# Optimization experiments

Measured on AMD Instinct MI355X. Metric: run time of the kernel, lower is better.

The kernel has to match this reference:

```python
import jax, jax.numpy as jnp
import numpy as np


def _conv2d(x, w, b):
    # x: [B,C,H,W], w: [O,I,kh,kw] (SAME padding, stride 1)
    y = jax.lax.conv_general_dilated(x, w, (1, 1), 'SAME',
                                     dimension_numbers=('NCHW', 'OIHW', 'NCHW'))
    return y + b[None, :, None, None]


def _conv1x1(x, w, b):
    # w: [O,C], b: [O]
    return jnp.einsum('oc,bchw->bohw', w, x) + b[None, :, None, None]


def _attention(xq, xkv, w, b):
    # w: [3,C,C] (q,k,v), b: [3,C]. Tokens = spatial positions, features = channels.
    B, C, H, W = xq.shape
    q = _conv1x1(xq, w[0], b[0]).reshape(B, C, H * W).transpose(0, 2, 1)   # [B,HW,C]
    k = _conv1x1(xkv, w[1], b[1]).reshape(B, C, H * W).transpose(0, 2, 1)
    v = _conv1x1(xkv, w[2], b[2]).reshape(B, C, H * W).transpose(0, 2, 1)
    scale = 1.0 / jnp.sqrt(jnp.asarray(C, xq.dtype))  # d_k = channels
    a = jax.nn.softmax(jnp.einsum('bnc,bmc->bnm', q, k) * scale, axis=-1)  # [B,HW,HW]
    out = jnp.einsum('bnm,bmc->bnc', a, v).transpose(0, 2, 1).reshape(B, C, H, W)
    return out + xq


def _cell(x, h, c, w, b):
    gates = _conv2d(jnp.concatenate([x, h], axis=1), w, b)
    i, f, o, g = jnp.split(gates, 4, axis=1)
    i, f, o, g = jax.nn.sigmoid(i), jax.nn.sigmoid(f), jax.nn.sigmoid(o), jnp.tanh(g)
    c_new = f * c + i * g
    h_new = o * jnp.tanh(c_new)
    return h_new, c_new


def setup_inputs() -> dict:
    key = jax.random.key(0)
    ks = iter(jax.random.split(key, 32))
    B, T, Cin, H, W = 2, 3, 1, 32, 32
    HID, L, K, OUT = 64, 2, 3, 1
    s = 0.02
    d = {
        'x1_seq': jax.random.normal(next(ks), (B, T, Cin, H, W), jnp.float32),
        'x2_seq': jax.random.normal(next(ks), (B, T, Cin, H, W), jnp.float32),
        # ConvLSTM gate convs: layer0 in = Cin+HID, layer1 in = 2*HID, per stream
        'conv1_w0': jax.random.normal(next(ks), (4 * HID, Cin + HID, K, K)) * s,
        'conv1_b0': jnp.zeros((4 * HID,)),
        'conv1_w1': jax.random.normal(next(ks), (4 * HID, 2 * HID, K, K)) * s,
        'conv1_b1': jnp.zeros((4 * HID,)),
        'conv2_w0': jax.random.normal(next(ks), (4 * HID, Cin + HID, K, K)) * s,
        'conv2_b0': jnp.zeros((4 * HID,)),
        'conv2_w1': jax.random.normal(next(ks), (4 * HID, 2 * HID, K, K)) * s,
        'conv2_b1': jnp.zeros((4 * HID,)),
        # attention 1x1 convs, stacked [L, 3(q/k/v), HID, HID]
        'sah_w': jax.random.normal(next(ks), (L, 3, HID, HID)) * s,
        'sah_b': jnp.zeros((L, 3, HID)),
        'sac_w': jax.random.normal(next(ks), (L, 3, HID, HID)) * s,
        'sac_b': jnp.zeros((L, 3, HID)),
        'cah_w': jax.random.normal(next(ks), (L, 3, HID, HID)) * s,
        'cah_b': jnp.zeros((L, 3, HID)),
        'cac_w': jax.random.normal(next(ks), (L, 3, HID, HID)) * s,
        'cac_b': jnp.zeros((L, 3, HID)),
        # decoder
        'dec_w1': jax.random.normal(next(ks), (HID, HID, 3, 3)) * s,
        'dec_b1': jnp.zeros((HID,)),
        'dec_w2': jax.random.normal(next(ks), (OUT, HID, 3, 3)) * s,
        'dec_b2': jnp.zeros((OUT,)),
        'future_steps': 4,
    }
    return d


def reference(x1_seq, x2_seq,
              conv1_w0, conv1_b0, conv1_w1, conv1_b1,
              conv2_w0, conv2_b0, conv2_w1, conv2_b1,
              sah_w, sah_b, sac_w, sac_b, cah_w, cah_b, cac_w, cac_b,
              dec_w1, dec_b1, dec_w2, dec_b2, future_steps):
    B, T, _, H, W = x1_seq.shape
    HID = sah_w.shape[-1]
    L = sah_w.shape[0]
    cw1 = [(conv1_w0, conv1_b0), (conv1_w1, conv1_b1)]
    cw2 = [(conv2_w0, conv2_b0), (conv2_w1, conv2_b1)]

    def decoder(h):
        return _conv2d(jax.nn.relu(_conv2d(h, dec_w1, dec_b1)), dec_w2, dec_b2)

    z = jnp.zeros((B, HID, H, W), x1_seq.dtype)
    h1s, c1s = [z] * L, [z] * L
    h2s, c2s = [z] * L, [z] * L

    def step(x1_t, x2_t, h1s, c1s, h2s, c2s):
        h1s, c1s, h2s, c2s = list(h1s), list(c1s), list(h2s), list(c2s)
        for l in range(L):
            h1, c1 = _cell(x1_t, h1s[l], c1s[l], *cw1[l])
            h2, c2 = _cell(x2_t, h2s[l], c2s[l], *cw2[l])
            h1 = _attention(h1, h1, sah_w[l], sah_b[l])
            c1 = _attention(c1, c1, sac_w[l], sac_b[l])
            h2 = _attention(h2, h2, sah_w[l], sah_b[l])
            c2 = _attention(c2, c2, sac_w[l], sac_b[l])
            tag_h1, tag_c1 = h1, c1
            h1 = _attention(h1, h2, cah_w[l], cah_b[l])
            c1 = _attention(c1, c2, cac_w[l], cac_b[l])
            h2 = _attention(h2, tag_h1, cah_w[l], cah_b[l])
            c2 = _attention(c2, tag_c1, cac_w[l], cac_b[l])
            h1s[l], c1s[l], h2s[l], c2s[l] = h1, c1, h2, c2
            x1_t, x2_t = h1, h2
        return h1s, c1s, h2s, c2s

    warm1, warm2 = [], []
    for t in range(T):
        h1s, c1s, h2s, c2s = step(x1_seq[:, t], x2_seq[:, t], h1s, c1s, h2s, c2s)
        if t < T - 1:
            warm1.append(h1s[-1])
            warm2.append(h2s[-1])
    pred_warm1 = jnp.stack([decoder(h) for h in warm1], axis=1)
    pred_warm2 = jnp.stack([decoder(h) for h in warm2], axis=1)

    preds1, preds2 = [], []
    for _ in range(int(future_steps)):
        p1 = decoder(h1s[-1])
        p2 = decoder(h2s[-1])
        preds1.append(p1)
        preds2.append(p2)
        h1s, c1s, h2s, c2s = step(p1, p2, h1s, c1s, h2s, c2s)
    preds1 = jnp.stack(preds1, axis=1)
    preds2 = jnp.stack(preds2, axis=1)
    return preds1, preds2, pred_warm1, pred_warm2
```

## Files before the change

kernel.cpp:

```cpp
#include <hip/hip_runtime.h>
#include <math.h>

#define BB 2
#define HIDC 64
#define HWN 1024

struct TWArgs { const float* src[5]; float* dst[5]; int icn9[5]; int osh[5]; };

__global__ __launch_bounds__(256) void transpose_w(TWArgs a) {
  const int arr = blockIdx.y;
  const int icn9 = a.icn9[arr], osh = a.osh[arr];
  const int ocn = 1 << osh;
  const float* s = a.src[arr];
  float* d = a.dst[arr];
  const int n = icn9 << osh;
  for (int i = blockIdx.x * 256 + threadIdx.x; i < n; i += gridDim.x * 256) {
    int oc = i & (ocn - 1), tt = i >> osh;
    d[i] = s[(size_t)oc * icn9 + tt];
  }
}

struct CellArgs {
  const float* x[2]; long xbs;
  const float* h[2]; const float* c[2];
  const float* w[2]; const float* bias[2];
  float* ho[2]; float* co[2];
};

template<int CX>
__global__ __launch_bounds__(512) void cell_kernel(CellArgs a) {
  constexpr int CT = CX + HIDC;
  constexpr int CH = (CT + 1) / 2;
  __shared__ float sIn[CT * 48];
  __shared__ float sGa[256 * 17];
  __shared__ float sGb[256 * 17];
  const int tile = blockIdx.x;
  const int b = blockIdx.y;
  const int st = blockIdx.z;
  const int ty0 = (tile >> 3) << 2, tx0 = (tile & 7) << 2;
  const float* xp = a.x[st] + (size_t)b * a.xbs;
  const float* hp = a.h[st] + (size_t)b * HIDC * HWN;

  for (int idx = threadIdx.x; idx < CT * 36; idx += 512) {
    int ic = idx / 36, pos = idx - ic * 36;
    int iy = pos / 6, ix = pos - iy * 6;
    int gy = ty0 - 1 + iy, gx = tx0 - 1 + ix;
    float v = 0.f;
    if ((unsigned)gy < 32u && (unsigned)gx < 32u) {
      v = (ic < CX) ? xp[ic * HWN + gy * 32 + gx]
                    : hp[(ic - CX) * HWN + gy * 32 + gx];
    }
    sIn[ic * 48 + iy * 8 + ix] = v;
  }
  __syncthreads();

  const int oc = threadIdx.x & 255;
  const int hh = threadIdx.x >> 8;
  const int icb = hh ? CH : 0, ice = hh ? CT : CH;
  float acc[16];
#pragma unroll
  for (int p = 0; p < 16; ++p) acc[p] = 0.f;
  const float* wp = a.w[st];
  for (int ic = icb; ic < ice; ++ic) {
    float w9[9];
#pragma unroll
    for (int t = 0; t < 9; ++t) w9[t] = wp[(ic * 9 + t) * 256 + oc];
    float in[36];
#pragma unroll
    for (int iy = 0; iy < 6; ++iy) {
      float4 v4 = *(const float4*)&sIn[ic * 48 + iy * 8];
      float2 v2 = *(const float2*)&sIn[ic * 48 + iy * 8 + 4];
      in[iy * 6 + 0] = v4.x; in[iy * 6 + 1] = v4.y; in[iy * 6 + 2] = v4.z;
      in[iy * 6 + 3] = v4.w; in[iy * 6 + 4] = v2.x; in[iy * 6 + 5] = v2.y;
    }
#pragma unroll
    for (int ky = 0; ky < 3; ++ky)
#pragma unroll
      for (int kx = 0; kx < 3; ++kx) {
        const float wv = w9[ky * 3 + kx];
#pragma unroll
        for (int py = 0; py < 4; ++py)
#pragma unroll
          for (int px = 0; px < 4; ++px)
            acc[py * 4 + px] += wv * in[(py + ky) * 6 + (px + kx)];
      }
  }
  float* sGh = hh ? sGb : sGa;
#pragma unroll
  for (int p = 0; p < 16; ++p) sGh[oc * 17 + p] = acc[p];
  __syncthreads();

  const float* cp = a.c[st] + (size_t)b * HIDC * HWN;
  float* hop = a.ho[st] + (size_t)b * HIDC * HWN;
  float* cop = a.co[st] + (size_t)b * HIDC * HWN;
  const float* bias = a.bias[st];
  for (int idx = threadIdx.x; idx < HIDC * 16; idx += 512) {
    int hc = idx >> 4, p = idx & 15;
    float gi = sGa[hc * 17 + p]         + sGb[hc * 17 + p]         + bias[hc];
    float gf = sGa[(hc + 64) * 17 + p]  + sGb[(hc + 64) * 17 + p]  + bias[hc + 64];
    float go = sGa[(hc + 128) * 17 + p] + sGb[(hc + 128) * 17 + p] + bias[hc + 128];
    float gg = sGa[(hc + 192) * 17 + p] + sGb[(hc + 192) * 17 + p] + bias[hc + 192];
    gi = 1.f / (1.f + expf(-gi));
    gf = 1.f / (1.f + expf(-gf));
    go = 1.f / (1.f + expf(-go));
    gg = tanhf(gg);
    int off = hc * HWN + (ty0 + (p >> 2)) * 32 + tx0 + (p & 3);
    float cn = gf * cp[off] + gi * gg;
    cop[off] = cn;
    hop[off] = go * tanhf(cn);
  }
}

struct QkvArgs {
  const float* xq[4]; const float* xkv[4];
  const float* w[4]; const float* bias[4];
  float* Q; float* K; float* V;
};

__global__ __launch_bounds__(256) void qkv_kernel(QkvArgs a) {
  __shared__ float sWt[64 * 68];
  const int ptile = blockIdx.x, b = blockIdx.y;
  const int attn = blockIdx.z / 3, proj = blockIdx.z % 3;
  const float* x = (proj == 0 ? a.xq[attn] : a.xkv[attn]) + (size_t)b * HIDC * HWN;
  const float* w = a.w[attn] + proj * 64 * 64;
  const float* bias = a.bias[attn] + proj * 64;
  float* dst = (proj == 0 ? a.Q : (proj == 1 ? a.K : a.V)) +
               ((size_t)attn * BB + b) * HWN * HIDC;
  for (int i = threadIdx.x; i < 4096; i += 256) {
    int o = i >> 6, c = i & 63;
    sWt[c * 68 + o] = w[i];
  }
  __syncthreads();
  const int pq = threadIdx.x & 63, og = threadIdx.x >> 6;
  const int p0 = ptile * 64 + pq;
  float acc[16];
#pragma unroll
  for (int k = 0; k < 16; ++k) acc[k] = bias[og * 16 + k];
  for (int c = 0; c < 64; ++c) {
    float xv = x[c * HWN + p0];
#pragma unroll
    for (int k = 0; k < 16; k += 4) {
      float4 wv = *(const float4*)&sWt[c * 68 + og * 16 + k];
      acc[k+0] += xv * wv.x; acc[k+1] += xv * wv.y;
      acc[k+2] += xv * wv.z; acc[k+3] += xv * wv.w;
    }
  }
  float* d = dst + (size_t)p0 * HIDC + og * 16;
#pragma unroll
  for (int k = 0; k < 16; k += 4) {
    float4 v; v.x = acc[k]; v.y = acc[k+1]; v.z = acc[k+2]; v.w = acc[k+3];
    *(float4*)&d[k] = v;
  }
}

struct AttnPArgs { const float* Q; const float* K; const float* V; float* pbuf; };

__global__ __launch_bounds__(256) void attn_part(AttnPArgs a) {
  __shared__ float sQt[64 * 64];
  __shared__ float sKt[64 * 64];
  __shared__ float sV [64 * 64];
  __shared__ float sPt[64 * 64];
  const int qt = blockIdx.x >> 2, ks = blockIdx.x & 3;
  const int b = blockIdx.y, at = blockIdx.z;
  const size_t base = ((size_t)at * BB + b) * HWN * HIDC;
  const float* Qp = a.Q + base + (size_t)qt * 64 * HIDC;
  const float* Kp = a.K + base;
  const float* Vp = a.V + base;
  const int tid = threadIdx.x;
  {
    const int qr = tid & 63, qc0 = (tid >> 6) * 16;
    const float* q = Qp + qr * HIDC + qc0;
#pragma unroll
    for (int k = 0; k < 16; k += 4) {
      float4 v = *(const float4*)&q[k];
      sQt[(qc0 + k + 0) * 64 + qr] = v.x * 0.125f;
      sQt[(qc0 + k + 1) * 64 + qr] = v.y * 0.125f;
      sQt[(qc0 + k + 2) * 64 + qr] = v.z * 0.125f;
      sQt[(qc0 + k + 3) * 64 + qr] = v.w * 0.125f;
    }
  }
  const int tc = tid & 15, tr = tid >> 4;
  const int j0 = tc * 4, r0 = tr * 4;
  const int kj = tid & 63, kch = (tid >> 6) * 16;
  const int vj = tid >> 2, vc0 = (tid & 3) * 16;
  float m[4], l[4], o[4][4];
#pragma unroll
  for (int i = 0; i < 4; ++i) {
    m[i] = -1e30f; l[i] = 0.f;
    o[i][0] = 0; o[i][1] = 0; o[i][2] = 0; o[i][3] = 0;
  }

  const int ktb = ks * 4;
  float4 kr[4], vr[4];
  {
    const float* kp = Kp + (size_t)(ktb * 64 + kj) * HIDC + kch;
    const float* vp = Vp + (size_t)(ktb * 64 + vj) * HIDC + vc0;
#pragma unroll
    for (int q2 = 0; q2 < 4; ++q2) {
      kr[q2] = *(const float4*)&kp[q2 * 4];
      vr[q2] = *(const float4*)&vp[q2 * 4];
    }
  }

  for (int kk = 0; kk < 4; ++kk) {
    __syncthreads();
#pragma unroll
    for (int q2 = 0; q2 < 4; ++q2) {
      sKt[(kch + q2 * 4 + 0) * 64 + kj] = kr[q2].x;
      sKt[(kch + q2 * 4 + 1) * 64 + kj] = kr[q2].y;
      sKt[(kch + q2 * 4 + 2) * 64 + kj] = kr[q2].z;
      sKt[(kch + q2 * 4 + 3) * 64 + kj] = kr[q2].w;
      int c = vc0 + q2 * 4;
      *(float4*)&sV[vj * 64 + (c ^ ((vj & 7) * 4))] = vr[q2];
    }
    __syncthreads();
    if (kk < 3) {
      const float* kp = Kp + (size_t)((ktb + kk + 1) * 64 + kj) * HIDC + kch;
      const float* vp = Vp + (size_t)((ktb + kk + 1) * 64 + vj) * HIDC + vc0;
#pragma unroll
      for (int q2 = 0; q2 < 4; ++q2) {
        kr[q2] = *(const float4*)&kp[q2 * 4];
        vr[q2] = *(const float4*)&vp[q2 * 4];
      }
    }
    float s[4][4];
#pragma unroll
    for (int i = 0; i < 4; ++i) { s[i][0]=0; s[i][1]=0; s[i][2]=0; s[i][3]=0; }
#pragma unroll 4
    for (int c = 0; c < 64; ++c) {
      float4 q4 = *(const float4*)&sQt[c * 64 + r0];
      float4 k4 = *(const float4*)&sKt[c * 64 + j0];
      s[0][0]+=q4.x*k4.x; s[0][1]+=q4.x*k4.y; s[0][2]+=q4.x*k4.z; s[0][3]+=q4.x*k4.w;
      s[1][0]+=q4.y*k4.x; s[1][1]+=q4.y*k4.y; s[1][2]+=q4.y*k4.z; s[1][3]+=q4.y*k4.w;
      s[2][0]+=q4.z*k4.x; s[2][1]+=q4.z*k4.y; s[2][2]+=q4.z*k4.z; s[2][3]+=q4.z*k4.w;
      s[3][0]+=q4.w*k4.x; s[3][1]+=q4.w*k4.y; s[3][2]+=q4.w*k4.z; s[3][3]+=q4.w*k4.w;
    }
    float mt[4];
#pragma unroll
    for (int i = 0; i < 4; ++i)
      mt[i] = fmaxf(fmaxf(s[i][0], s[i][1]), fmaxf(s[i][2], s[i][3]));
#pragma unroll
    for (int d = 1; d < 16; d <<= 1) {
#pragma unroll
      for (int i = 0; i < 4; ++i) mt[i] = fmaxf(mt[i], __shfl_xor(mt[i], d));
    }
    float al[4];
#pragma unroll
    for (int i = 0; i < 4; ++i) {
      float mn = fmaxf(m[i], mt[i]);
      al[i] = __expf(m[i] - mn);
      m[i] = mn;
      s[i][0] = __expf(s[i][0] - mn); s[i][1] = __expf(s[i][1] - mn);
      s[i][2] = __expf(s[i][2] - mn); s[i][3] = __expf(s[i][3] - mn);
    }
    float ps[4];
#pragma unroll
    for (int i = 0; i < 4; ++i) ps[i] = s[i][0] + s[i][1] + s[i][2] + s[i][3];
#pragma unroll
    for (int d = 1; d < 16; d <<= 1) {
#pragma unroll
      for (int i = 0; i < 4; ++i) ps[i] += __shfl_xor(ps[i], d);
    }
#pragma unroll
    for (int i = 0; i < 4; ++i) {
      l[i] = l[i] * al[i] + ps[i];
      o[i][0] *= al[i]; o[i][1] *= al[i]; o[i][2] *= al[i]; o[i][3] *= al[i];
    }
#pragma unroll
    for (int jj = 0; jj < 4; ++jj) {
      int j = j0 + jj;
      float4 pv; pv.x = s[0][jj]; pv.y = s[1][jj]; pv.z = s[2][jj]; pv.w = s[3][jj];
      *(float4*)&sPt[j * 64 + (r0 ^ ((j & 7) * 4))] = pv;
    }
    __syncthreads();
#pragma unroll 4
    for (int j = 0; j < 64; ++j) {
      float4 p4 = *(const float4*)&sPt[j * 64 + (r0 ^ ((j & 7) * 4))];
      float4 v4 = *(const float4*)&sV [j * 64 + (j0 ^ ((j & 7) * 4))];
      o[0][0]+=p4.x*v4.x; o[0][1]+=p4.x*v4.y; o[0][2]+=p4.x*v4.z; o[0][3]+=p4.x*v4.w;
      o[1][0]+=p4.y*v4.x; o[1][1]+=p4.y*v4.y; o[1][2]+=p4.y*v4.z; o[1][3]+=p4.y*v4.w;
      o[2][0]+=p4.z*v4.x; o[2][1]+=p4.z*v4.y; o[2][2]+=p4.z*v4.z; o[2][3]+=p4.z*v4.w;
      o[3][0]+=p4.w*v4.x; o[3][1]+=p4.w*v4.y; o[3][2]+=p4.w*v4.z; o[3][3]+=p4.w*v4.w;
    }
  }
  float* pb = a.pbuf + ((((size_t)at * BB + b) * 16 + qt) * 4 + ks) * 4224;
#pragma unroll
  for (int i = 0; i < 4; ++i) {
    float4 w; w.x = o[i][0]; w.y = o[i][1]; w.z = o[i][2]; w.w = o[i][3];
    *(float4*)&pb[(r0 + i) * 64 + j0] = w;
  }
  if (tc == 0) {
#pragma unroll
    for (int i = 0; i < 4; ++i) {
      pb[4096 + r0 + i] = m[i];
      pb[4160 + r0 + i] = l[i];
    }
  }
}

struct AttnMArgs { const float* pbuf; const float* xq[4]; float* out[4]; };

__global__ __launch_bounds__(256) void attn_merge(AttnMArgs a) {
  __shared__ float sW[4][64];
  __shared__ float sL[64];
  const int qt = blockIdx.x, b = blockIdx.y, at = blockIdx.z;
  const float* pb = a.pbuf + (((size_t)at * BB + b) * 16 + qt) * 4 * 4224;
  if (threadIdx.x < 64) {
    int r = threadIdx.x;
    float m0 = pb[4096 + r],          m1 = pb[4224 + 4096 + r];
    float m2 = pb[2*4224 + 4096 + r], m3 = pb[3*4224 + 4096 + r];
    float M = fmaxf(fmaxf(m0, m1), fmaxf(m2, m3));
    float w0 = __expf(m0 - M), w1 = __expf(m1 - M);
    float w2 = __expf(m2 - M), w3 = __expf(m3 - M);
    sW[0][r] = w0; sW[1][r] = w1; sW[2][r] = w2; sW[3][r] = w3;
    sL[r] = pb[4160 + r] * w0 + pb[4224 + 4160 + r] * w1 +
            pb[2*4224 + 4160 + r] * w2 + pb[3*4224 + 4160 + r] * w3;
  }
  __syncthreads();
  const int c = threadIdx.x >> 2, rg = (threadIdx.x & 3) * 16;
  const float* xq = a.xq[at] + (size_t)b * HIDC * HWN;
  float* op = a.out[at] + (size_t)b * HIDC * HWN;
  const int p0 = qt * 64 + rg;
#pragma unroll
  for (int rr4 = 0; rr4 < 16; rr4 += 4) {
    float rv[4];
#pragma unroll
    for (int k = 0; k < 4; ++k) {
      int r = rg + rr4 + k;
      float acc = pb[r*64 + c] * sW[0][r] + pb[4224 + r*64 + c] * sW[1][r]
                + pb[2*4224 + r*64 + c] * sW[2][r] + pb[3*4224 + r*64 + c] * sW[3][r];
      rv[k] = acc / sL[r];
    }
    float4 x4 = *(const float4*)&xq[(size_t)c * HWN + p0 + rr4];
    float4 res; res.x = rv[0] + x4.x; res.y = rv[1] + x4.y;
    res.z = rv[2] + x4.z; res.w = rv[3] + x4.w;
    *(float4*)&op[(size_t)c * HWN + p0 + rr4] = res;
  }
}

struct Dec1Args { const float* in[2]; const float* w; const float* b; float* tmp; };

__global__ __launch_bounds__(512) void dec1_kernel(Dec1Args a) {
  __shared__ float sIn[64 * 48];
  __shared__ float sHa[64 * 17];
  __shared__ float sHb[64 * 17];
  const int tile = blockIdx.x, b = blockIdx.y, st = blockIdx.z;
  const int ty0 = (tile >> 3) << 2, tx0 = (tile & 7) << 2;
  const float* ip = a.in[st] + (size_t)b * HIDC * HWN;
  for (int idx = threadIdx.x; idx < 64 * 36; idx += 512) {
    int ic = idx / 36, pos = idx - ic * 36;
    int iy = pos / 6, ix = pos - iy * 6;
    int gy = ty0 - 1 + iy, gx = tx0 - 1 + ix;
    float v = 0.f;
    if ((unsigned)gy < 32u && (unsigned)gx < 32u) v = ip[ic * HWN + gy * 32 + gx];
    sIn[ic * 48 + iy * 8 + ix] = v;
  }
  __syncthreads();
  const int oc = threadIdx.x & 63, ps = (threadIdx.x >> 6) & 3;
  const int hh = threadIdx.x >> 8;
  const int icb = hh * 32, ice = icb + 32;
  float acc0 = 0.f, acc1 = 0.f, acc2 = 0.f, acc3 = 0.f;
  const float* wp = a.w;
  for (int ic = icb; ic < ice; ++ic) {
    float w9[9];
#pragma unroll
    for (int t = 0; t < 9; ++t) w9[t] = wp[(ic * 9 + t) * 64 + oc];
    float in[18];
#pragma unroll
    for (int ry = 0; ry < 3; ++ry) {
      float4 v4 = *(const float4*)&sIn[ic * 48 + (ps + ry) * 8];
      float2 v2 = *(const float2*)&sIn[ic * 48 + (ps + ry) * 8 + 4];
      in[ry*6+0]=v4.x; in[ry*6+1]=v4.y; in[ry*6+2]=v4.z; in[ry*6+3]=v4.w;
      in[ry*6+4]=v2.x; in[ry*6+5]=v2.y;
    }
#pragma unroll
    for (int ky = 0; ky < 3; ++ky)
#pragma unroll
      for (int kx = 0; kx < 3; ++kx) {
        float wv = w9[ky * 3 + kx];
        acc0 += wv * in[ky * 6 + kx + 0];
        acc1 += wv * in[ky * 6 + kx + 1];
        acc2 += wv * in[ky * 6 + kx + 2];
        acc3 += wv * in[ky * 6 + kx + 3];
      }
  }
  float* sH = hh ? sHb : sHa;
  sH[oc * 17 + ps * 4 + 0] = acc0;
  sH[oc * 17 + ps * 4 + 1] = acc1;
  sH[oc * 17 + ps * 4 + 2] = acc2;
  sH[oc * 17 + ps * 4 + 3] = acc3;
  __syncthreads();
  float* dst = a.tmp + ((size_t)st * BB + b) * HIDC * HWN;
  for (int idx = threadIdx.x; idx < 1024; idx += 512) {
    int oc2 = idx >> 4, p = idx & 15;
    float v = sHa[oc2 * 17 + p] + sHb[oc2 * 17 + p] + a.b[oc2];
    v = fmaxf(v, 0.f);
    dst[(size_t)oc2 * HWN + (ty0 + (p >> 2)) * 32 + tx0 + (p & 3)] = v;
  }
}

struct Dec2Args { const float* tmp; const float* w; const float* b;
                  float* dst0; float* dst1; long bstr; };

__global__ __launch_bounds__(256) void dec2_kernel(Dec2Args a) {
  __shared__ float sIn[64 * 48];
  __shared__ float sW[64 * 9];
  const int tile = blockIdx.x, b = blockIdx.y, st = blockIdx.z;
  const int ty0 = (tile >> 3) << 2, tx0 = (tile & 7) << 2;
  const float* ip = a.tmp + ((size_t)st * BB + b) * HIDC * HWN;
  for (int idx = threadIdx.x; idx < 64 * 36; idx += 256) {
    int ic = idx / 36, pos = idx - ic * 36;
    int iy = pos / 6, ix = pos - iy * 6;
    int gy = ty0 - 1 + iy, gx = tx0 - 1 + ix;
    float v = 0.f;
    if ((unsigned)gy < 32u && (unsigned)gx < 32u) v = ip[ic * HWN + gy * 32 + gx];
    sIn[ic * 48 + iy * 8 + ix] = v;
  }
  for (int idx = threadIdx.x; idx < 576; idx += 256) sW[idx] = a.w[idx];
  __syncthreads();
  const int px = threadIdx.x >> 4, icg = threadIdx.x & 15;
  const int py = px >> 2, pxx = px & 3;
  float acc = 0.f;
#pragma unroll
  for (int i = 0; i < 4; ++i) {
    int ic = icg * 4 + i;
    const float* row = &sIn[ic * 48];
    const float* wv = &sW[ic * 9];
#pragma unroll
    for (int ky = 0; ky < 3; ++ky)
#pragma unroll
      for (int kx = 0; kx < 3; ++kx)
        acc += wv[ky * 3 + kx] * row[(py + ky) * 8 + pxx + kx];
  }
#pragma unroll
  for (int d = 1; d < 16; d <<= 1) acc += __shfl_xor(acc, d);
  if (icg == 0) {
    float* d = (st == 0 ? a.dst0 : a.dst1);
    d[(size_t)b * a.bstr + (ty0 + py) * 32 + tx0 + pxx] = acc + a.b[0];
  }
}

extern "C" void kernel_launch(void* const* d_in, const int* in_sizes, int n_in,
                              void* d_out, int out_size, void* d_ws, size_t ws_size,
                              hipStream_t stream) {
  (void)in_sizes; (void)n_in; (void)out_size; (void)ws_size;
  const float* x1_seq = (const float*)d_in[0];
  const float* x2_seq = (const float*)d_in[1];
  const float* c1w[2] = {(const float*)d_in[2], (const float*)d_in[4]};
  const float* c1b[2] = {(const float*)d_in[3], (const float*)d_in[5]};
  const float* c2w[2] = {(const float*)d_in[6], (const float*)d_in[8]};
  const float* c2b[2] = {(const float*)d_in[7], (const float*)d_in[9]};
  const float* sah_w = (const float*)d_in[10]; const float* sah_b = (const float*)d_in[11];
  const float* sac_w = (const float*)d_in[12]; const float* sac_b = (const float*)d_in[13];
  const float* cah_w = (const float*)d_in[14]; const float* cah_b = (const float*)d_in[15];
  const float* cac_w = (const float*)d_in[16]; const float* cac_b = (const float*)d_in[17];
  const float* dw1 = (const float*)d_in[18]; const float* db1 = (const float*)d_in[19];
  const float* dw2 = (const float*)d_in[20]; const float* db2 = (const float*)d_in[21];
  float* out = (float*)d_out;
  float* ws = (float*)d_ws;

  const size_t SPL = (size_t)BB * HIDC * HWN;
  float* h1s = ws;
  float* c1s = h1s + 2 * SPL;
  float* h2s = c1s + 2 * SPL;
  float* c2s = h2s + 2 * SPL;
  float* hc1 = c2s + 2 * SPL;
  float* cc1 = hc1 + SPL;
  float* hc2 = cc1 + SPL;
  float* cc2 = hc2 + SPL;
  float* hs1 = cc2 + SPL;
  float* cs1 = hs1 + SPL;
  float* hs2 = cs1 + SPL;
  float* cs2 = hs2 + SPL;
  float* Qb  = cs2 + SPL;
  float* Kb  = Qb + 4 * SPL;
  float* Vb  = Kb + 4 * SPL;
  float* dtmp = Vb + 4 * SPL;
  float* pbuf = dtmp + 2 * SPL;
  float* wt10 = pbuf + (size_t)4 * BB * 16 * 4 * 4224;
  float* wt11 = wt10 + 585 * 256;
  float* wt20 = wt11 + 1152 * 256;
  float* wt21 = wt20 + 585 * 256;
  float* wtd  = wt21 + 1152 * 256;

  hipMemsetAsync(ws, 0, 8 * SPL * sizeof(float), stream);

  const dim3 blk(256);
  const dim3 blk2(512);

  {
    TWArgs tw;
    tw.src[0] = c1w[0]; tw.dst[0] = wt10; tw.icn9[0] = 585;  tw.osh[0] = 8;
    tw.src[1] = c1w[1]; tw.dst[1] = wt11; tw.icn9[1] = 1152; tw.osh[1] = 8;
    tw.src[2] = c2w[0]; tw.dst[2] = wt20; tw.icn9[2] = 585;  tw.osh[2] = 8;
    tw.src[3] = c2w[1]; tw.dst[3] = wt21; tw.icn9[3] = 1152; tw.osh[3] = 8;
    tw.src[4] = dw1;    tw.dst[4] = wtd;  tw.icn9[4] = 576;  tw.osh[4] = 6;
    transpose_w<<<dim3(32, 5), blk, 0, stream>>>(tw);
  }

  auto attn_stage = [&](const float* q0, const float* q1, const float* q2, const float* q3,
                        const float* k0, const float* k1, const float* k2, const float* k3,
                        const float* wh, const float* bh, const float* wc, const float* bc,
                        float* o0, float* o1, float* o2, float* o3) {
    QkvArgs qa;
    qa.xq[0]=q0; qa.xq[1]=q1; qa.xq[2]=q2; qa.xq[3]=q3;
    qa.xkv[0]=k0; qa.xkv[1]=k1; qa.xkv[2]=k2; qa.xkv[3]=k3;
    qa.w[0]=wh; qa.w[1]=wc; qa.w[2]=wh; qa.w[3]=wc;
    qa.bias[0]=bh; qa.bias[1]=bc; qa.bias[2]=bh; qa.bias[3]=bc;
    qa.Q=Qb; qa.K=Kb; qa.V=Vb;
    qkv_kernel<<<dim3(16, BB, 12), blk, 0, stream>>>(qa);
    AttnPArgs ap; ap.Q=Qb; ap.K=Kb; ap.V=Vb; ap.pbuf=pbuf;
    attn_part<<<dim3(64, BB, 4), blk, 0, stream>>>(ap);
    AttnMArgs am; am.pbuf=pbuf;
    am.xq[0]=q0; am.xq[1]=q1; am.xq[2]=q2; am.xq[3]=q3;
    am.out[0]=o0; am.out[1]=o1; am.out[2]=o2; am.out[3]=o3;
    attn_merge<<<dim3(16, BB, 4), blk, 0, stream>>>(am);
  };

  auto decode = [&](long off1, long off2, long bstr) {
    Dec1Args d1; d1.in[0] = h1s + SPL; d1.in[1] = h2s + SPL;
    d1.w = wtd; d1.b = db1; d1.tmp = dtmp;
    dec1_kernel<<<dim3(64, BB, 2), blk2, 0, stream>>>(d1);
    Dec2Args d2; d2.tmp = dtmp; d2.w = dw2; d2.b = db2;
    d2.dst0 = out + off1; d2.dst1 = out + off2; d2.bstr = bstr;
    dec2_kernel<<<dim3(64, BB, 2), blk, 0, stream>>>(d2);
  };

  for (int s = 0; s < 6; ++s) {
    const float *x1, *x2; long xbs;
    if (s < 3) { x1 = x1_seq + s * HWN; x2 = x2_seq + s * HWN; xbs = 3 * HWN; }
    else       { x1 = out + (s - 3) * HWN; x2 = out + 8192 + (s - 3) * HWN; xbs = 4 * HWN; }

    for (int l = 0; l < 2; ++l) {
      if (l == 1) { x1 = h1s; x2 = h2s; xbs = (long)HIDC * HWN; }
      CellArgs ca;
      ca.x[0] = x1; ca.x[1] = x2; ca.xbs = xbs;
      ca.h[0] = h1s + l * SPL; ca.h[1] = h2s + l * SPL;
      ca.c[0] = c1s + l * SPL; ca.c[1] = c2s + l * SPL;
      ca.w[0] = (l == 0) ? wt10 : wt11;
      ca.w[1] = (l == 0) ? wt20 : wt21;
      ca.bias[0] = c1b[l]; ca.bias[1] = c2b[l];
      ca.ho[0] = hc1; ca.ho[1] = hc2; ca.co[0] = cc1; ca.co[1] = cc2;
      if (l == 0) cell_kernel<1><<<dim3(64, BB, 2), blk2, 0, stream>>>(ca);
      else        cell_kernel<64><<<dim3(64, BB, 2), blk2, 0, stream>>>(ca);

      attn_stage(hc1, cc1, hc2, cc2,
                 hc1, cc1, hc2, cc2,
                 sah_w + l * 12288, sah_b + l * 192,
                 sac_w + l * 12288, sac_b + l * 192,
                 hs1, cs1, hs2, cs2);
      attn_stage(hs1, cs1, hs2, cs2,
                 hs2, cs2, hs1, cs1,
                 cah_w + l * 12288, cah_b + l * 192,
                 cac_w + l * 12288, cac_b + l * 192,
                 h1s + l * SPL, c1s + l * SPL, h2s + l * SPL, c2s + l * SPL);
    }

    if (s == 0)      decode(16384,        20480,        2048);
    else if (s == 1) decode(16384 + 1024, 20480 + 1024, 2048);
    else             decode((s - 2) * HWN, 8192 + (s - 2) * HWN, 4096);
  }
}
```

Baseline: 2.432 ms.

## Store K channel-major and read K/V from global in attention, double KV splits

```diff
diff --git a/kernel.cpp b/kernel.cpp
--- a/kernel.cpp
+++ b/kernel.cpp
@@ -124,8 +124,7 @@
   const float* x = (proj == 0 ? a.xq[attn] : a.xkv[attn]) + (size_t)b * HIDC * HWN;
   const float* w = a.w[attn] + proj * 64 * 64;
   const float* bias = a.bias[attn] + proj * 64;
-  float* dst = (proj == 0 ? a.Q : (proj == 1 ? a.K : a.V)) +
-               ((size_t)attn * BB + b) * HWN * HIDC;
+  const size_t bb = (size_t)attn * BB + b;
   for (int i = threadIdx.x; i < 4096; i += 256) {
     int o = i >> 6, c = i & 63;
     sWt[c * 68 + o] = w[i];
@@ -145,27 +144,33 @@
       acc[k+2] += xv * wv.z; acc[k+3] += xv * wv.w;
     }
   }
-  float* d = dst + (size_t)p0 * HIDC + og * 16;
-#pragma unroll
-  for (int k = 0; k < 16; k += 4) {
-    float4 v; v.x = acc[k]; v.y = acc[k+1]; v.z = acc[k+2]; v.w = acc[k+3];
-    *(float4*)&d[k] = v;
-  }
-}
-
-struct AttnPArgs { const float* Q; const float* K; const float* V; float* pbuf; };
+  if (proj == 1) {
+    float* dK = a.K + bb * HIDC * HWN;
+#pragma unroll
+    for (int k = 0; k < 16; ++k)
+      dK[(size_t)(og * 16 + k) * HWN + p0] = acc[k];
+  } else {
+    float* dst = (proj == 0 ? a.Q : a.V) + bb * HWN * HIDC;
+    float* d = dst + (size_t)p0 * HIDC + og * 16;
+#pragma unroll
+    for (int k = 0; k < 16; k += 4) {
+      float4 v; v.x = acc[k]; v.y = acc[k+1]; v.z = acc[k+2]; v.w = acc[k+3];
+      *(float4*)&d[k] = v;
+    }
+  }
+}
+
+struct AttnPArgs { const float* Q; const float* Kt; const float* V; float* pbuf; };
 
 __global__ __launch_bounds__(256) void attn_part(AttnPArgs a) {
   __shared__ float sQt[64 * 64];
-  __shared__ float sKt[64 * 64];
-  __shared__ float sV [64 * 64];
   __shared__ float sPt[64 * 64];
-  const int qt = blockIdx.x >> 2, ks = blockIdx.x & 3;
+  const int qt = blockIdx.x >> 3, ks = blockIdx.x & 7;
   const int b = blockIdx.y, at = blockIdx.z;
-  const size_t base = ((size_t)at * BB + b) * HWN * HIDC;
-  const float* Qp = a.Q + base + (size_t)qt * 64 * HIDC;
-  const float* Kp = a.K + base;
-  const float* Vp = a.V + base;
+  const size_t bb = (size_t)at * BB + b;
+  const float* Qp  = a.Q  + bb * HWN * HIDC + (size_t)qt * 64 * HIDC;
+  const float* Ktp = a.Kt + bb * HIDC * HWN;
+  const float* Vp  = a.V  + bb * HWN * HIDC;
   const int tid = threadIdx.x;
   {
     const int qr = tid & 63, qc0 = (tid >> 6) * 16;
@@ -181,55 +186,24 @@
   }
   const int tc = tid & 15, tr = tid >> 4;
   const int j0 = tc * 4, r0 = tr * 4;
-  const int kj = tid & 63, kch = (tid >> 6) * 16;
-  const int vj = tid >> 2, vc0 = (tid & 3) * 16;
   float m[4], l[4], o[4][4];
 #pragma unroll
   for (int i = 0; i < 4; ++i) {
     m[i] = -1e30f; l[i] = 0.f;
     o[i][0] = 0; o[i][1] = 0; o[i][2] = 0; o[i][3] = 0;
   }
-
-  const int ktb = ks * 4;
-  float4 kr[4], vr[4];
-  {
-    const float* kp = Kp + (size_t)(ktb * 64 + kj) * HIDC + kch;
-    const float* vp = Vp + (size_t)(ktb * 64 + vj) * HIDC + vc0;
-#pragma unroll
-    for (int q2 = 0; q2 < 4; ++q2) {
-      kr[q2] = *(const float4*)&kp[q2 * 4];
-      vr[q2] = *(const float4*)&vp[q2 * 4];
-    }
-  }
-
-  for (int kk = 0; kk < 4; ++kk) {
-    __syncthreads();
-#pragma unroll
-    for (int q2 = 0; q2 < 4; ++q2) {
-      sKt[(kch + q2 * 4 + 0) * 64 + kj] = kr[q2].x;
-      sKt[(kch + q2 * 4 + 1) * 64 + kj] = kr[q2].y;
-      sKt[(kch + q2 * 4 + 2) * 64 + kj] = kr[q2].z;
-      sKt[(kch + q2 * 4 + 3) * 64 + kj] = kr[q2].w;
-      int c = vc0 + q2 * 4;
-      *(float4*)&sV[vj * 64 + (c ^ ((vj & 7) * 4))] = vr[q2];
-    }
-    __syncthreads();
-    if (kk < 3) {
-      const float* kp = Kp + (size_t)((ktb + kk + 1) * 64 + kj) * HIDC + kch;
-      const float* vp = Vp + (size_t)((ktb + kk + 1) * 64 + vj) * HIDC + vc0;
-#pragma unroll
-      for (int q2 = 0; q2 < 4; ++q2) {
-        kr[q2] = *(const float4*)&kp[q2 * 4];
-        vr[q2] = *(const float4*)&vp[q2 * 4];
-      }
-    }
+  __syncthreads();
+
+  for (int kk = 0; kk < 2; ++kk) {
+    const int jg = (ks * 2 + kk) * 64;
     float s[4][4];
 #pragma unroll
     for (int i = 0; i < 4; ++i) { s[i][0]=0; s[i][1]=0; s[i][2]=0; s[i][3]=0; }
-#pragma unroll 4
+    const float* kp = Ktp + jg + j0;
+#pragma unroll 8
     for (int c = 0; c < 64; ++c) {
       float4 q4 = *(const float4*)&sQt[c * 64 + r0];
-      float4 k4 = *(const float4*)&sKt[c * 64 + j0];
+      float4 k4 = *(const float4*)&kp[(size_t)c * HWN];
       s[0][0]+=q4.x*k4.x; s[0][1]+=q4.x*k4.y; s[0][2]+=q4.x*k4.z; s[0][3]+=q4.x*k4.w;
       s[1][0]+=q4.y*k4.x; s[1][1]+=q4.y*k4.y; s[1][2]+=q4.y*k4.z; s[1][3]+=q4.y*k4.w;
       s[2][0]+=q4.z*k4.x; s[2][1]+=q4.z*k4.y; s[2][2]+=q4.z*k4.z; s[2][3]+=q4.z*k4.w;
@@ -266,6 +240,7 @@
       l[i] = l[i] * al[i] + ps[i];
       o[i][0] *= al[i]; o[i][1] *= al[i]; o[i][2] *= al[i]; o[i][3] *= al[i];
     }
+    __syncthreads();
 #pragma unroll
     for (int jj = 0; jj < 4; ++jj) {
       int j = j0 + jj;
@@ -273,17 +248,18 @@
       *(float4*)&sPt[j * 64 + (r0 ^ ((j & 7) * 4))] = pv;
     }
     __syncthreads();
-#pragma unroll 4
+    const float* vp = Vp + (size_t)jg * HIDC + j0;
+#pragma unroll 8
     for (int j = 0; j < 64; ++j) {
       float4 p4 = *(const float4*)&sPt[j * 64 + (r0 ^ ((j & 7) * 4))];
-      float4 v4 = *(const float4*)&sV [j * 64 + (j0 ^ ((j & 7) * 4))];
+      float4 v4 = *(const float4*)&vp[(size_t)j * HIDC];
       o[0][0]+=p4.x*v4.x; o[0][1]+=p4.x*v4.y; o[0][2]+=p4.x*v4.z; o[0][3]+=p4.x*v4.w;
       o[1][0]+=p4.y*v4.x; o[1][1]+=p4.y*v4.y; o[1][2]+=p4.y*v4.z; o[1][3]+=p4.y*v4.w;
       o[2][0]+=p4.z*v4.x; o[2][1]+=p4.z*v4.y; o[2][2]+=p4.z*v4.z; o[2][3]+=p4.z*v4.w;
       o[3][0]+=p4.w*v4.x; o[3][1]+=p4.w*v4.y; o[3][2]+=p4.w*v4.z; o[3][3]+=p4.w*v4.w;
     }
   }
-  float* pb = a.pbuf + ((((size_t)at * BB + b) * 16 + qt) * 4 + ks) * 4224;
+  float* pb = a.pbuf + ((bb * 16 + qt) * 8 + ks) * 4224;
 #pragma unroll
   for (int i = 0; i < 4; ++i) {
     float4 w; w.x = o[i][0]; w.y = o[i][1]; w.z = o[i][2]; w.w = o[i][3];
@@ -301,20 +277,26 @@
 struct AttnMArgs { const float* pbuf; const float* xq[4]; float* out[4]; };
 
 __global__ __launch_bounds__(256) void attn_merge(AttnMArgs a) {
-  __shared__ float sW[4][64];
+  __shared__ float sW[8][64];
   __shared__ float sL[64];
   const int qt = blockIdx.x, b = blockIdx.y, at = blockIdx.z;
-  const float* pb = a.pbuf + (((size_t)at * BB + b) * 16 + qt) * 4 * 4224;
+  const float* pb = a.pbuf + (((size_t)at * BB + b) * 16 + qt) * 8 * 4224;
   if (threadIdx.x < 64) {
     int r = threadIdx.x;
-    float m0 = pb[4096 + r],          m1 = pb[4224 + 4096 + r];
-    float m2 = pb[2*4224 + 4096 + r], m3 = pb[3*4224 + 4096 + r];
-    float M = fmaxf(fmaxf(m0, m1), fmaxf(m2, m3));
-    float w0 = __expf(m0 - M), w1 = __expf(m1 - M);
-    float w2 = __expf(m2 - M), w3 = __expf(m3 - M);
-    sW[0][r] = w0; sW[1][r] = w1; sW[2][r] = w2; sW[3][r] = w3;
-    sL[r] = pb[4160 + r] * w0 + pb[4224 + 4160 + r] * w1 +
-            pb[2*4224 + 4160 + r] * w2 + pb[3*4224 + 4160 + r] * w3;
+    float mm[8];
+#pragma unroll
+    for (int i = 0; i < 8; ++i) mm[i] = pb[i * 4224 + 4096 + r];
+    float M = mm[0];
+#pragma unroll
+    for (int i = 1; i < 8; ++i) M = fmaxf(M, mm[i]);
+    float L = 0.f;
+#pragma unroll
+    for (int i = 0; i < 8; ++i) {
+      float w = __expf(mm[i] - M);
+      sW[i][r] = w;
+      L += pb[i * 4224 + 4160 + r] * w;
+    }
+    sL[r] = L;
   }
   __syncthreads();
   const int c = threadIdx.x >> 2, rg = (threadIdx.x & 3) * 16;
@@ -327,8 +309,9 @@
 #pragma unroll
     for (int k = 0; k < 4; ++k) {
       int r = rg + rr4 + k;
-      float acc = pb[r*64 + c] * sW[0][r] + pb[4224 + r*64 + c] * sW[1][r]
-                + pb[2*4224 + r*64 + c] * sW[2][r] + pb[3*4224 + r*64 + c] * sW[3][r];
+      float acc = 0.f;
+#pragma unroll
+      for (int i = 0; i < 8; ++i) acc += pb[i * 4224 + r * 64 + c] * sW[i][r];
       rv[k] = acc / sL[r];
     }
     float4 x4 = *(const float4*)&xq[(size_t)c * HWN + p0 + rr4];
@@ -477,7 +460,7 @@
   float* Vb  = Kb + 4 * SPL;
   float* dtmp = Vb + 4 * SPL;
   float* pbuf = dtmp + 2 * SPL;
-  float* wt10 = pbuf + (size_t)4 * BB * 16 * 4 * 4224;
+  float* wt10 = pbuf + (size_t)4 * BB * 16 * 8 * 4224;
   float* wt11 = wt10 + 585 * 256;
   float* wt20 = wt11 + 1152 * 256;
   float* wt21 = wt20 + 585 * 256;
@@ -509,8 +492,8 @@
     qa.bias[0]=bh; qa.bias[1]=bc; qa.bias[2]=bh; qa.bias[3]=bc;
     qa.Q=Qb; qa.K=Kb; qa.V=Vb;
     qkv_kernel<<<dim3(16, BB, 12), blk, 0, stream>>>(qa);
-    AttnPArgs ap; ap.Q=Qb; ap.K=Kb; ap.V=Vb; ap.pbuf=pbuf;
-    attn_part<<<dim3(64, BB, 4), blk, 0, stream>>>(ap);
+    AttnPArgs ap; ap.Q=Qb; ap.Kt=Kb; ap.V=Vb; ap.pbuf=pbuf;
+    attn_part<<<dim3(128, BB, 4), blk, 0, stream>>>(ap);
     AttnMArgs am; am.pbuf=pbuf;
     am.xq[0]=q0; am.xq[1]=q1; am.xq[2]=q2; am.xq[3]=q3;
     am.out[0]=o0; am.out[1]=o1; am.out[2]=o2; am.out[3]=o3;
```

After: 2.527 ms. 3.9% more time.
